# Kernel optimization log

Measured on AMD Instinct MI355X. Metric: run time of the kernel, lower is better.

The kernel has to match this reference:

```python
import jax, jax.numpy as jnp
import numpy as np

B, N, D = 4, 1024, 1024
H, DK, DV = 8, 128, 128
EPS = 1e-6


def setup_inputs() -> dict:
    key = jax.random.key(0)
    ks = jax.random.split(key, 16)
    s = 0.02
    return {
        "q_time": jax.random.normal(ks[0], (B, N, D), jnp.float32),
        "k_time": jax.random.normal(ks[1], (B, N, D), jnp.float32),
        "q_feature": jax.random.normal(ks[2], (B, N, D), jnp.float32),
        "k_feature": jax.random.normal(ks[3], (B, N, D), jnp.float32),
        "v": jax.random.normal(ks[4], (B, N, D), jnp.float32),
        "attn_mask": jax.random.randint(ks[5], (B, N, N), 0, 2, jnp.int32),
        "w_qs_time": jax.random.normal(ks[6], (H * DK, D), jnp.float32) * s,
        "w_ks_time": jax.random.normal(ks[7], (H * DK, D), jnp.float32) * s,
        "w_qs_feature": jax.random.normal(ks[8], (H * DV, D), jnp.float32) * s,
        "w_ks_feature": jax.random.normal(ks[9], (H * DV, D), jnp.float32) * s,
        "w_vs": jax.random.normal(ks[10], (H * DV, D), jnp.float32) * s,
        "w_fc": jax.random.normal(ks[11], (D, H * DV), jnp.float32) * s,
        "ln_gamma": jnp.ones((D,), jnp.float32),
        "ln_beta": jnp.zeros((D,), jnp.float32),
    }


def reference(q_time, k_time, q_feature, k_feature, v, attn_mask,
              w_qs_time, w_ks_time, w_qs_feature, w_ks_feature, w_vs,
              w_fc, ln_gamma, ln_beta):
    temp = DK ** 0.5
    residual = v

    def proj(x, w, d):
        # [B,N,D] @ [D, H*d] -> [B,H,N,d]
        return (x @ w.T).reshape(B, N, H, d).transpose(0, 2, 1, 3)

    qt = proj(q_time, w_qs_time, DK)
    kt = proj(k_time, w_ks_time, DK)
    qf = proj(q_feature, w_qs_feature, DV)
    kf = proj(k_feature, w_ks_feature, DV)
    vv = proj(v, w_vs, DV)

    # time attention: [B,H,N,N]
    attn_time = jnp.einsum('bhnd,bhmd->bhnm', qt / temp, kt)
    attn_time = jnp.where(attn_mask[:, None, :, :] == 0, -1e9, attn_time)
    attn_time = jax.nn.softmax(attn_time, axis=-1)

    # feature attention: q_feature^T @ k_feature -> [B,H,DV,DV]
    attn_feature = jnp.einsum('bhnd,bhne->bhde', qf / temp, kf)
    attn_feature = jax.nn.softmax(attn_feature, axis=-1)

    # chained matmuls: (attn_time @ v) @ attn_feature -> [B,H,N,DV]
    out = jnp.einsum('bhnm,bhmd->bhnd', attn_time, vv)
    out = jnp.einsum('bhnd,bhde->bhne', out, attn_feature)

    out = out.transpose(0, 2, 1, 3).reshape(B, N, H * DV)
    out = out @ w_fc.T + residual  # dropout = identity (eval)

    mean = jnp.mean(out, axis=-1, keepdims=True)
    var = jnp.var(out, axis=-1, keepdims=True)
    out = (out - mean) / jnp.sqrt(var + EPS) * ln_gamma + ln_beta
    return out, attn_time, attn_feature
```

## Files before the change

### kernel.cpp

```cpp
#include <hip/hip_runtime.h>
#include <hip/hip_bf16.h>
#include <cstdint>
#include <cstddef>

typedef unsigned short u16;
typedef unsigned int u32;
typedef short v8s __attribute__((ext_vector_type(8)));
typedef float v4f __attribute__((ext_vector_type(4)));
typedef __hip_bfloat16 bf16;

#define PROJ_ELEMS  4194304ull
#define AT_ELEMS    33554432ull
#define INV_TEMP    0.08838834764831845f

#define GLOBAL_AS __attribute__((address_space(1)))
#define LDS_AS    __attribute__((address_space(3)))

__device__ __forceinline__ void store_out(float* p, float v) { *p = v; }
__device__ __forceinline__ void store_out(bf16* p, float v) { *p = __float2bfloat16(v); }

__device__ __forceinline__ v8s load8f(const float* p) {
    const float4 a = *(const float4*)p;
    const float4 b = *(const float4*)(p + 4);
    v8s r;
    bf16 t;
    t = __float2bfloat16(a.x); r[0] = *(const short*)&t;
    t = __float2bfloat16(a.y); r[1] = *(const short*)&t;
    t = __float2bfloat16(a.z); r[2] = *(const short*)&t;
    t = __float2bfloat16(a.w); r[3] = *(const short*)&t;
    t = __float2bfloat16(b.x); r[4] = *(const short*)&t;
    t = __float2bfloat16(b.y); r[5] = *(const short*)&t;
    t = __float2bfloat16(b.z); r[6] = *(const short*)&t;
    t = __float2bfloat16(b.w); r[7] = *(const short*)&t;
    return r;
}

template <typename AT, typename OutT>
__device__ __forceinline__ void gemm_core(
    const AT* __restrict__ Ab, const u16* __restrict__ Bb, OutT* __restrict__ Cb,
    int K, int lda, int ldb, int ldc, float alpha, int m0, int n0)
{
    __shared__ __align__(16) u16 sA[128][32];
    __shared__ __align__(16) u16 sB[128][32];

    const int tid  = threadIdx.x;
    const int lane = tid & 63;
    const int wid  = tid >> 6;
    const int wm = (wid >> 1) * 64;
    const int wn = (wid & 1) * 64;
    const int quad = lane >> 4;
    const int l16  = lane & 15;

    v4f acc[4][4];
    #pragma unroll
    for (int i = 0; i < 4; ++i)
        #pragma unroll
        for (int j = 0; j < 4; ++j)
            acc[i][j] = (v4f){0.f, 0.f, 0.f, 0.f};

    for (int k0 = 0; k0 < K; k0 += 32) {
        #pragma unroll
        for (int it = 0; it < 2; ++it) {
            const int slot = tid + it * 256;
            const int row  = slot >> 2;
            const int cg   = (slot & 3) << 3;
            __builtin_amdgcn_global_load_lds(
                (const GLOBAL_AS void*)(Bb + (size_t)(n0 + row) * (size_t)ldb + (size_t)(k0 + cg)),
                (LDS_AS void*)((char*)&sB[0][0] + slot * 16), 16, 0, 0);
            if constexpr (sizeof(AT) == 2) {
                __builtin_amdgcn_global_load_lds(
                    (const GLOBAL_AS void*)((const u16*)Ab + (size_t)(m0 + row) * (size_t)lda + (size_t)(k0 + cg)),
                    (LDS_AS void*)((char*)&sA[0][0] + slot * 16), 16, 0, 0);
            } else {
                *(v8s*)&sA[row][cg] =
                    load8f((const float*)Ab + (size_t)(m0 + row) * (size_t)lda + (size_t)(k0 + cg));
            }
        }
        __syncthreads();

        v8s af[4], bfr[4];
        #pragma unroll
        for (int i = 0; i < 4; ++i) {
            af[i]  = *(const v8s*)&sA[wm + i * 16 + l16][quad * 8];
            bfr[i] = *(const v8s*)&sB[wn + i * 16 + l16][quad * 8];
        }
        #pragma unroll
        for (int i = 0; i < 4; ++i)
            #pragma unroll
            for (int j = 0; j < 4; ++j)
                acc[i][j] = __builtin_amdgcn_mfma_f32_16x16x32_bf16(af[i], bfr[j], acc[i][j], 0, 0, 0);
        __syncthreads();
    }

    #pragma unroll
    for (int i = 0; i < 4; ++i) {
        int rbase = m0 + wm + i * 16 + quad * 4;
        #pragma unroll
        for (int j = 0; j < 4; ++j) {
            int gcol = n0 + wn + j * 16 + l16;
            #pragma unroll
            for (int r = 0; r < 4; ++r)
                store_out(&Cb[(size_t)(rbase + r) * (size_t)ldc + (size_t)gcol],
                          acc[i][j][r] * alpha);
        }
    }
}

template <typename AT, typename OutT>
__global__ __launch_bounds__(256, 2)
void gemm_fast(const AT* __restrict__ A, const u16* __restrict__ B, OutT* __restrict__ C,
               int K, int lda, int ldb, int ldc, int batDiv,
               long long sAo, long long sAi, long long sBo, long long sBi,
               long long sCo, long long sCi, float alpha)
{
    const int z  = blockIdx.z;
    const int zo = z / batDiv;
    const int zi = z - zo * batDiv;
    gemm_core<AT, OutT>(A + (size_t)zo * (size_t)sAo + (size_t)zi * (size_t)sAi,
                        B + (size_t)zo * (size_t)sBo + (size_t)zi * (size_t)sBi,
                        C + (size_t)zo * (size_t)sCo + (size_t)zi * (size_t)sCi,
                        K, lda, ldb, ldc, alpha, blockIdx.y * 128, blockIdx.x * 128);
}

struct P5 { const u16* a[5]; };
__global__ __launch_bounds__(256, 2)
void gemm_proj5(P5 As, const u16* __restrict__ W, u16* __restrict__ C)
{
    const int z = blockIdx.z;
    gemm_core<u16, bf16>(As.a[z], W + (size_t)z * 1048576ull,
                         (bf16*)(C + (size_t)z * PROJ_ELEMS),
                         1024, 1024, 1024, 1024, 1.f, blockIdx.y * 128, blockIdx.x * 128);
}

__global__ __launch_bounds__(256, 2)
void gemm_feat_sk(const u16* __restrict__ qfT, const u16* __restrict__ kfT, float* __restrict__ Fp)
{
    const int kc = blockIdx.x, z = blockIdx.y;
    gemm_core<u16, float>(qfT + (size_t)z * 131072ull + (size_t)kc * 128ull,
                          kfT + (size_t)z * 131072ull + (size_t)kc * 128ull,
                          Fp + ((size_t)kc * 32 + z) * 16384ull,
                          128, 1024, 1024, 128, INV_TEMP, 0, 0);
}

template <int NT> struct CP { const float* p[NT]; };

template <int NT>
__global__ __launch_bounds__(256)
void cvt_batch(CP<NT> ps, u16* __restrict__ dst, int perElems)
{
    const float* s = ps.p[blockIdx.z];
    u16* d = dst + (size_t)blockIdx.z * (size_t)perElems;
    const int i = (blockIdx.x * 256 + threadIdx.x) * 8;
    *(v8s*)(d + i) = load8f(s + i);
}

__global__ __launch_bounds__(256)
void mask_pack(const int* __restrict__ mask, u32* __restrict__ mb)
{
    const int w = blockIdx.x * 256 + threadIdx.x;
    const int* src = mask + (size_t)w * 32ull;
    u32 bits = 0;
    #pragma unroll
    for (int i = 0; i < 32; i += 4) {
        int4 v = *(const int4*)(src + i);
        bits |= (u32)(v.x != 0) << i;
        bits |= (u32)(v.y != 0) << (i + 1);
        bits |= (u32)(v.z != 0) << (i + 2);
        bits |= (u32)(v.w != 0) << (i + 3);
    }
    mb[w] = bits;
}

struct T3 { const u16* in[3]; u16* out[3]; };
__global__ __launch_bounds__(256)
void transpose3(T3 t3)
{
    __shared__ u16 tile[32][33];
    const int sel = blockIdx.z >> 5;
    const int z   = blockIdx.z & 31;
    const int b = z >> 3, h = z & 7;
    const u16* ib = t3.in[sel] + (size_t)b * 1048576ull + (size_t)h * 128ull;
    u16* ob = t3.out[sel] + (size_t)z * 131072ull;
    const int m0 = blockIdx.x * 32;
    const int d0 = blockIdx.y * 32;
    const int tx = threadIdx.x;
    const int ty = threadIdx.y;
    #pragma unroll
    for (int i = 0; i < 4; ++i)
        tile[ty + i * 8][tx] = ib[(size_t)(m0 + ty + i * 8) * 1024ull + (size_t)(d0 + tx)];
    __syncthreads();
    #pragma unroll
    for (int i = 0; i < 4; ++i)
        ob[(size_t)(d0 + ty + i * 8) * 1024ull + (size_t)(m0 + tx)] = tile[tx][ty + i * 8];
}

__global__ __launch_bounds__(256, 1)
void fused_attn(const u16* __restrict__ qt, const u16* __restrict__ kt,
                const u16* __restrict__ vvT, const u32* __restrict__ mb,
                float* __restrict__ oAT, u16* __restrict__ opv)
{
    __shared__ __align__(16) u16 sQ[4][128][32];
    __shared__ __align__(16) u16 sK[128][32];
    __shared__ __align__(16) u16 sV[128][32];
    __shared__ __align__(16) u16 sP[4][128][32];
    __shared__ float Mld[128], Lld[128], redT[128];
    __shared__ u32 smw[128][4];

    const int z = blockIdx.y;
    const int b = z >> 3, h = z & 7;
    const int m0 = blockIdx.x * 128;
    const u16* qb = qt + (size_t)b * 1048576ull + (size_t)h * 128ull;
    const u16* kb = kt + (size_t)b * 1048576ull + (size_t)h * 128ull;
    const u16* vb = vvT + (size_t)z * 131072ull;
    float* Ob = oAT + (size_t)z * 1048576ull;
    const u32* mbb = mb + (size_t)b * 32768ull;

    const int tid = threadIdx.x;
    const int lane = tid & 63, wid = tid >> 6;
    const int wm = (wid >> 1) * 64, wn = (wid & 1) * 64;
    const int quad = lane >> 4, l16 = lane & 15;
    const int wnw = wn >> 5;

    if (tid < 128) { Mld[tid] = -3.0e38f; Lld[tid] = 0.f; }

    #pragma unroll
    for (int ks = 0; ks < 4; ++ks)
        #pragma unroll
        for (int it = 0; it < 2; ++it) {
            const int slot = tid + it * 256;
            const int row = slot >> 2, cg = (slot & 3) << 3;
            __builtin_amdgcn_global_load_lds(
                (const GLOBAL_AS void*)(qb + (size_t)(m0 + row) * 1024ull + ks * 32 + cg),
                (LDS_AS void*)((char*)&sQ[ks][0][0] + slot * 16), 16, 0, 0);
        }

    for (int nt = 0; nt < 8; ++nt) {
        v4f acc[4][4];
        #pragma unroll
        for (int i = 0; i < 4; ++i)
            #pragma unroll
            for (int j = 0; j < 4; ++j)
                acc[i][j] = (v4f){0.f, 0.f, 0.f, 0.f};

        #pragma unroll
        for (int ks = 0; ks < 4; ++ks) {
            #pragma unroll
            for (int it = 0; it < 2; ++it) {
                const int slot = tid + it * 256;
                const int row = slot >> 2, cg = (slot & 3) << 3;
                __builtin_amdgcn_global_load_lds(
                    (const GLOBAL_AS void*)(kb + (size_t)(nt * 128 + row) * 1024ull + ks * 32 + cg),
                    (LDS_AS void*)((char*)&sK[0][0] + slot * 16), 16, 0, 0);
            }
            __syncthreads();
            v8s af[4], bfr[4];
            #pragma unroll
            for (int i = 0; i < 4; ++i) {
                af[i]  = *(const v8s*)&sQ[ks][wm + i * 16 + l16][quad * 8];
                bfr[i] = *(const v8s*)&sK[wn + i * 16 + l16][quad * 8];
            }
            #pragma unroll
            for (int i = 0; i < 4; ++i)
                #pragma unroll
                for (int j = 0; j < 4; ++j)
                    acc[i][j] = __builtin_amdgcn_mfma_f32_16x16x32_bf16(af[i], bfr[j], acc[i][j], 0, 0, 0);
            __syncthreads();
        }

        {
            const int row = tid >> 1, w0 = (tid & 1) * 2;
            *(uint2*)&smw[row][w0] = *(const uint2*)(mbb + (size_t)(m0 + row) * 32ull + nt * 4 + w0);
        }
        __syncthreads();

        float tm[4][4];
        #pragma unroll
        for (int i = 0; i < 4; ++i)
            #pragma unroll
            for (int r = 0; r < 4; ++r) {
                tm[i][r] = -3.0e38f;
                const int rowl = wm + i * 16 + quad * 4 + r;
                #pragma unroll
                for (int j = 0; j < 4; ++j) {
                    const u32 word = smw[rowl][wnw + (j >> 1)];
                    const int bit = ((j & 1) << 4) + l16;
                    float s = acc[i][j][r] * INV_TEMP;
                    s = ((word >> bit) & 1u) ? s : -1e9f;
                    acc[i][j][r] = s;
                    tm[i][r] = fmaxf(tm[i][r], s);
                }
                #pragma unroll
                for (int m = 1; m <= 8; m <<= 1)
                    tm[i][r] = fmaxf(tm[i][r], __shfl_xor(tm[i][r], m));
            }

        if ((wid & 1) && l16 == 0) {
            #pragma unroll
            for (int i = 0; i < 4; ++i)
                #pragma unroll
                for (int r = 0; r < 4; ++r)
                    redT[wm + i * 16 + quad * 4 + r] = tm[i][r];
        }
        __syncthreads();

        float scl[4][4];
        if (!(wid & 1) && l16 == 0) {
            #pragma unroll
            for (int i = 0; i < 4; ++i)
                #pragma unroll
                for (int r = 0; r < 4; ++r) {
                    const int rowl = wm + i * 16 + quad * 4 + r;
                    const float full = fmaxf(tm[i][r], redT[rowl]);
                    const float oldM = Mld[rowl];
                    const float newM = fmaxf(oldM, full);
                    Mld[rowl] = newM;
                    scl[i][r] = __expf(oldM - newM);
                }
        }
        __syncthreads();

        float ts[4][4];
        #pragma unroll
        for (int i = 0; i < 4; ++i)
            #pragma unroll
            for (int r = 0; r < 4; ++r) {
                const int rowl = wm + i * 16 + quad * 4 + r;
                const float Mv = Mld[rowl];
                float t = 0.f;
                #pragma unroll
                for (int j = 0; j < 4; ++j)
                    t += __expf(acc[i][j][r] - Mv);
                #pragma unroll
                for (int m = 1; m <= 8; m <<= 1)
                    t += __shfl_xor(t, m);
                ts[i][r] = t;
            }
        if ((wid & 1) && l16 == 0) {
            #pragma unroll
            for (int i = 0; i < 4; ++i)
                #pragma unroll
                for (int r = 0; r < 4; ++r)
                    redT[wm + i * 16 + quad * 4 + r] = ts[i][r];
        }
        __syncthreads();
        if (!(wid & 1) && l16 == 0) {
            #pragma unroll
            for (int i = 0; i < 4; ++i)
                #pragma unroll
                for (int r = 0; r < 4; ++r) {
                    const int rowl = wm + i * 16 + quad * 4 + r;
                    Lld[rowl] = Lld[rowl] * scl[i][r] + ts[i][r] + redT[rowl];
                }
        }
        __syncthreads();
    }

    float Mr[16], IL[16];
    #pragma unroll
    for (int i = 0; i < 4; ++i)
        #pragma unroll
        for (int r = 0; r < 4; ++r) {
            const int rowl = wm + i * 16 + quad * 4 + r;
            Mr[i * 4 + r] = Mld[rowl];
            IL[i * 4 + r] = 1.f / Lld[rowl];
        }

    v4f pacc[4][4];
    #pragma unroll
    for (int i = 0; i < 4; ++i)
        #pragma unroll
        for (int j = 0; j < 4; ++j)
            pacc[i][j] = (v4f){0.f, 0.f, 0.f, 0.f};

    for (int nt = 0; nt < 8; ++nt) {
        v4f acc[4][4];
        #pragma unroll
        for (int i = 0; i < 4; ++i)
            #pragma unroll
            for (int j = 0; j < 4; ++j)
                acc[i][j] = (v4f){0.f, 0.f, 0.f, 0.f};

        #pragma unroll
        for (int ks = 0; ks < 4; ++ks) {
            #pragma unroll
            for (int it = 0; it < 2; ++it) {
                const int slot = tid + it * 256;
                const int row = slot >> 2, cg = (slot & 3) << 3;
                __builtin_amdgcn_global_load_lds(
                    (const GLOBAL_AS void*)(kb + (size_t)(nt * 128 + row) * 1024ull + ks * 32 + cg),
                    (LDS_AS void*)((char*)&sK[0][0] + slot * 16), 16, 0, 0);
            }
            __syncthreads();
            v8s af[4], bfr[4];
            #pragma unroll
            for (int i = 0; i < 4; ++i) {
                af[i]  = *(const v8s*)&sQ[ks][wm + i * 16 + l16][quad * 8];
                bfr[i] = *(const v8s*)&sK[wn + i * 16 + l16][quad * 8];
            }
            #pragma unroll
            for (int i = 0; i < 4; ++i)
                #pragma unroll
                for (int j = 0; j < 4; ++j)
                    acc[i][j] = __builtin_amdgcn_mfma_f32_16x16x32_bf16(af[i], bfr[j], acc[i][j], 0, 0, 0);
            __syncthreads();
        }

        {
            const int row = tid >> 1, w0 = (tid & 1) * 2;
            *(uint2*)&smw[row][w0] = *(const uint2*)(mbb + (size_t)(m0 + row) * 32ull + nt * 4 + w0);
        }
        __syncthreads();

        #pragma unroll
        for (int i = 0; i < 4; ++i)
            #pragma unroll
            for (int r = 0; r < 4; ++r) {
                const int rowl = wm + i * 16 + quad * 4 + r;
                const int idx = i * 4 + r;
                #pragma unroll
                for (int j = 0; j < 4; ++j) {
                    const u32 word = smw[rowl][wnw + (j >> 1)];
                    const int bit = ((j & 1) << 4) + l16;
                    float s = acc[i][j][r] * INV_TEMP;
                    s = ((word >> bit) & 1u) ? s : -1e9f;
                    const float p = __expf(s - Mr[idx]) * IL[idx];
                    const int c = wn + j * 16 + l16;
                    Ob[(size_t)(m0 + rowl) * 1024ull + nt * 128 + c] = p;
                    bf16 pb = __float2bfloat16(p);
                    sP[c >> 5][rowl][c & 31] = *(const u16*)&pb;
                }
            }
        __syncthreads();

        #pragma unroll
        for (int ks = 0; ks < 4; ++ks) {
            #pragma unroll
            for (int it = 0; it < 2; ++it) {
                const int slot = tid + it * 256;
                const int row = slot >> 2, cg = (slot & 3) << 3;
                __builtin_amdgcn_global_load_lds(
                    (const GLOBAL_AS void*)(vb + (size_t)row * 1024ull + nt * 128 + ks * 32 + cg),
                    (LDS_AS void*)((char*)&sV[0][0] + slot * 16), 16, 0, 0);
            }
            __syncthreads();
            v8s af[4], bfr[4];
            #pragma unroll
            for (int i = 0; i < 4; ++i) {
                af[i]  = *(const v8s*)&sP[ks][wm + i * 16 + l16][quad * 8];
                bfr[i] = *(const v8s*)&sV[wn + i * 16 + l16][quad * 8];
            }
            #pragma unroll
            for (int i = 0; i < 4; ++i)
                #pragma unroll
                for (int j = 0; j < 4; ++j)
                    pacc[i][j] = __builtin_amdgcn_mfma_f32_16x16x32_bf16(af[i], bfr[j], pacc[i][j], 0, 0, 0);
            __syncthreads();
        }
    }

    u16* opvB = opv + (size_t)z * 131072ull;
    #pragma unroll
    for (int i = 0; i < 4; ++i) {
        const int rbase = m0 + wm + i * 16 + quad * 4;
        #pragma unroll
        for (int j = 0; j < 4; ++j) {
            const int e = wn + j * 16 + l16;
            #pragma unroll
            for (int r = 0; r < 4; ++r) {
                bf16 t = __float2bfloat16(pacc[i][j][r]);
                opvB[(size_t)(rbase + r) * 128ull + e] = *(const u16*)&t;
            }
        }
    }
}

__global__ __launch_bounds__(128)
void softmax_feat(const float* __restrict__ Fp, float* __restrict__ out_af, u16* __restrict__ FT)
{
    const int r = blockIdx.x;
    const int z = r >> 7, d = r & 127;
    const int e = threadIdx.x;
    float x = 0.f;
    #pragma unroll
    for (int kc = 0; kc < 8; ++kc)
        x += Fp[((size_t)kc * 32 + z) * 16384ull + (size_t)d * 128ull + e];
    float mx = x;
    #pragma unroll
    for (int o = 32; o; o >>= 1) mx = fmaxf(mx, __shfl_xor(mx, o));
    __shared__ float redm[2], reds[2];
    const int w = e >> 6;
    if ((e & 63) == 0) redm[w] = mx;
    __syncthreads();
    mx = fmaxf(redm[0], redm[1]);
    float ex = __expf(x - mx);
    float s = ex;
    #pragma unroll
    for (int o = 32; o; o >>= 1) s += __shfl_xor(s, o);
    if ((e & 63) == 0) reds[w] = s;
    __syncthreads();
    s = reds[0] + reds[1];
    float p = ex / s;
    out_af[(size_t)r * 128ull + e] = p;
    bf16 pb = __float2bfloat16(p);
    FT[(size_t)z * 16384ull + (size_t)e * 128ull + d] = *(const u16*)&pb;
}

__global__ __launch_bounds__(256)
void resid_ln(const float* __restrict__ fc, const float* __restrict__ v,
              const float* __restrict__ gamma, const float* __restrict__ beta,
              float* __restrict__ out)
{
    const int r = blockIdx.x;
    const int t = threadIdx.x;
    const float4* fr = (const float4*)(fc + (size_t)r * 1024ull);
    const float4* vr = (const float4*)(v  + (size_t)r * 1024ull);
    float4 a = fr[t], b4 = vr[t];
    float4 x = {a.x + b4.x, a.y + b4.y, a.z + b4.z, a.w + b4.w};
    float s  = x.x + x.y + x.z + x.w;
    float s2 = x.x * x.x + x.y * x.y + x.z * x.z + x.w * x.w;
    #pragma unroll
    for (int o = 32; o; o >>= 1) { s += __shfl_xor(s, o); s2 += __shfl_xor(s2, o); }
    __shared__ float rs[4], rs2[4];
    const int w = t >> 6;
    if ((t & 63) == 0) { rs[w] = s; rs2[w] = s2; }
    __syncthreads();
    s  = rs[0] + rs[1] + rs[2] + rs[3];
    s2 = rs2[0] + rs2[1] + rs2[2] + rs2[3];
    const float mean = s * (1.f / 1024.f);
    const float var  = s2 * (1.f / 1024.f) - mean * mean;
    const float rstd = rsqrtf(var + 1e-6f);
    const float4 g = ((const float4*)gamma)[t];
    const float4 bb = ((const float4*)beta)[t];
    float4 o4 = {(x.x - mean) * rstd * g.x + bb.x,
                 (x.y - mean) * rstd * g.y + bb.y,
                 (x.z - mean) * rstd * g.z + bb.z,
                 (x.w - mean) * rstd * g.w + bb.w};
    ((float4*)(out + (size_t)r * 1024ull))[t] = o4;
}

extern "C" void kernel_launch(void* const* d_in, const int* in_sizes, int n_in,
                              void* d_out, int out_size, void* d_ws, size_t ws_size,
                              hipStream_t stream)
{
    (void)in_sizes; (void)n_in; (void)out_size; (void)ws_size;
    const float* q_time    = (const float*)d_in[0];
    const float* k_time    = (const float*)d_in[1];
    const float* q_feature = (const float*)d_in[2];
    const float* k_feature = (const float*)d_in[3];
    const float* v_in      = (const float*)d_in[4];
    const int*   mask      = (const int*)d_in[5];
    const float* w_qs_t    = (const float*)d_in[6];
    const float* w_ks_t    = (const float*)d_in[7];
    const float* w_qs_f    = (const float*)d_in[8];
    const float* w_ks_f    = (const float*)d_in[9];
    const float* w_vs      = (const float*)d_in[10];
    const float* w_fc      = (const float*)d_in[11];
    const float* gamma     = (const float*)d_in[12];
    const float* beta      = (const float*)d_in[13];

    char* ws = (char*)d_ws;
    const size_t MB = 1ull << 20;
    u16*   act = (u16*)(ws + 0  * MB);
    u16*   wbf = (u16*)(ws + 40 * MB);
    u16*   qt  = (u16*)(ws + 52 * MB);
    u16*   vvT = (u16*)(ws + 0  * MB);
    u16*   qfT = (u16*)(ws + 8  * MB);
    u16*   kfT = (u16*)(ws + 16 * MB);
    u16*   FT  = (u16*)(ws + 24 * MB);
    float* Fp  = (float*)(ws + 25 * MB);
    u16*   opv = (u16*)(ws + 41 * MB);
    u16*   o2  = (u16*)(ws + 52 * MB);
    float* fc  = (float*)(ws + 60 * MB);
    u32*   mb  = (u32*)(ws + 92 * MB);
    u16*   kt  = qt + PROJ_ELEMS;
    u16*   qf  = kt + PROJ_ELEMS;
    u16*   kf  = qf + PROJ_ELEMS;
    u16*   vv  = kf + PROJ_ELEMS;
    u16*   wfc = wbf + 5ull * 1048576ull;

    float* out0 = (float*)d_out;
    float* oAT  = out0 + PROJ_ELEMS;
    float* oAF  = out0 + PROJ_ELEMS + AT_ELEMS;

    const dim3 blk(256);

    {
        CP<5> ca; ca.p[0] = q_time; ca.p[1] = k_time; ca.p[2] = q_feature;
                  ca.p[3] = k_feature; ca.p[4] = v_in;
        cvt_batch<5><<<dim3(2048, 1, 5), blk, 0, stream>>>(ca, act, 4194304);
        CP<6> cw; cw.p[0] = w_qs_t; cw.p[1] = w_ks_t; cw.p[2] = w_qs_f;
                  cw.p[3] = w_ks_f; cw.p[4] = w_vs; cw.p[5] = w_fc;
        cvt_batch<6><<<dim3(512, 1, 6), blk, 0, stream>>>(cw, wbf, 1048576);
        mask_pack<<<512, blk, 0, stream>>>(mask, mb);
    }

    {
        P5 ps; for (int i = 0; i < 5; ++i) ps.a[i] = act + (size_t)i * PROJ_ELEMS;
        gemm_proj5<<<dim3(8, 32, 5), blk, 0, stream>>>(ps, wbf, qt);
    }

    {
        T3 t3; t3.in[0] = vv; t3.in[1] = qf; t3.in[2] = kf;
               t3.out[0] = vvT; t3.out[1] = qfT; t3.out[2] = kfT;
        transpose3<<<dim3(32, 4, 96), dim3(32, 8, 1), 0, stream>>>(t3);
    }

    gemm_feat_sk<<<dim3(8, 32), blk, 0, stream>>>(qfT, kfT, Fp);

    softmax_feat<<<4096, 128, 0, stream>>>(Fp, oAF, FT);

    fused_attn<<<dim3(8, 32), blk, 0, stream>>>(qt, kt, vvT, mb, oAT, opv);

    gemm_fast<<<dim3(1, 8, 32), blk, 0, stream>>>(opv, FT, (bf16*)o2, 128,
        128, 128, 1024, 8, 1048576LL, 131072LL, 131072LL, 16384LL, 1048576LL, 128LL, 1.f);

    gemm_fast<<<dim3(8, 32, 1), blk, 0, stream>>>(o2, wfc, fc, 1024, 1024, 1024, 1024, 1,
        0LL, 0LL, 0LL, 0LL, 0LL, 0LL, 1.f);

    resid_ln<<<4096, 256, 0, stream>>>(fc, v_in, gamma, beta, out0);
}
```

Baseline: 493.3 us.

## Double-buffer K/V/mask tiles and give each wave full rows for register softmax

```diff
diff --git a/kernel.cpp b/kernel.cpp
--- a/kernel.cpp
+++ b/kernel.cpp
@@ -200,11 +200,9 @@
                 float* __restrict__ oAT, u16* __restrict__ opv)
 {
     __shared__ __align__(16) u16 sQ[4][128][32];
-    __shared__ __align__(16) u16 sK[128][32];
-    __shared__ __align__(16) u16 sV[128][32];
-    __shared__ __align__(16) u16 sP[4][128][32];
-    __shared__ float Mld[128], Lld[128], redT[128];
-    __shared__ u32 smw[128][4];
+    __shared__ __align__(16) u16 sT[2][4][128][32];
+    __shared__ __align__(16) u16 sP[4][128][40];
+    __shared__ u32 smw[2][128][4];
 
     const int z = blockIdx.y;
     const int b = z >> 3, h = z & 7;
@@ -217,254 +215,237 @@
 
     const int tid = threadIdx.x;
     const int lane = tid & 63, wid = tid >> 6;
-    const int wm = (wid >> 1) * 64, wn = (wid & 1) * 64;
     const int quad = lane >> 4, l16 = lane & 15;
-    const int wnw = wn >> 5;
-
-    if (tid < 128) { Mld[tid] = -3.0e38f; Lld[tid] = 0.f; }
-
-    #pragma unroll
-    for (int ks = 0; ks < 4; ++ks)
+    const int wm = wid * 32;
+
+    auto stK = [&](int nt, int buf) {
+        #pragma unroll
+        for (int it = 0; it < 8; ++it) {
+            const int slot = tid + it * 256;
+            const int ks = slot >> 9, row = (slot >> 2) & 127, cg = (slot & 3) << 3;
+            __builtin_amdgcn_global_load_lds(
+                (const GLOBAL_AS void*)(kb + (size_t)(nt * 128 + row) * 1024ull + ks * 32 + cg),
+                (LDS_AS void*)((char*)&sT[buf][0][0][0] + slot * 16), 16, 0, 0);
+        }
+    };
+    auto stV = [&](int nt, int buf) {
+        #pragma unroll
+        for (int it = 0; it < 8; ++it) {
+            const int slot = tid + it * 256;
+            const int ks = slot >> 9, row = (slot >> 2) & 127, cg = (slot & 3) << 3;
+            __builtin_amdgcn_global_load_lds(
+                (const GLOBAL_AS void*)(vb + (size_t)row * 1024ull + nt * 128 + ks * 32 + cg),
+                (LDS_AS void*)((char*)&sT[buf][0][0][0] + slot * 16), 16, 0, 0);
+        }
+    };
+    auto stM = [&](int nt, int buf) {
         #pragma unroll
         for (int it = 0; it < 2; ++it) {
-            const int slot = tid + it * 256;
-            const int row = slot >> 2, cg = (slot & 3) << 3;
+            const int W = wid * 128 + it * 64 + lane;
             __builtin_amdgcn_global_load_lds(
-                (const GLOBAL_AS void*)(qb + (size_t)(m0 + row) * 1024ull + ks * 32 + cg),
-                (LDS_AS void*)((char*)&sQ[ks][0][0] + slot * 16), 16, 0, 0);
-        }
-
+                (const GLOBAL_AS void*)(mbb + (size_t)(m0 + (W >> 2)) * 32ull + nt * 4 + (W & 3)),
+                (LDS_AS void*)((char*)&smw[buf][0][0] + W * 4), 4, 0, 0);
+        }
+    };
+
+    #pragma unroll
+    for (int it = 0; it < 8; ++it) {
+        const int slot = tid + it * 256;
+        const int ks = slot >> 9, row = (slot >> 2) & 127, cg = (slot & 3) << 3;
+        __builtin_amdgcn_global_load_lds(
+            (const GLOBAL_AS void*)(qb + (size_t)(m0 + row) * 1024ull + ks * 32 + cg),
+            (LDS_AS void*)((char*)&sQ[0][0][0] + slot * 16), 16, 0, 0);
+    }
+    stK(0, 0); stM(0, 0);
+
+    float Mreg[8], Lreg[8];
+    #pragma unroll
+    for (int x = 0; x < 8; ++x) { Mreg[x] = -3.0e38f; Lreg[x] = 0.f; }
+
+    int bufA = 0, mcur = 0;
     for (int nt = 0; nt < 8; ++nt) {
-        v4f acc[4][4];
-        #pragma unroll
-        for (int i = 0; i < 4; ++i)
-            #pragma unroll
-            for (int j = 0; j < 4; ++j)
+        stK((nt + 1) & 7, bufA ^ 1);
+        stM((nt + 1) & 7, mcur ^ 1);
+        asm volatile("s_waitcnt vmcnt(10)" ::: "memory");
+        __builtin_amdgcn_s_barrier();
+        __builtin_amdgcn_sched_barrier(0);
+
+        v4f acc[2][8];
+        #pragma unroll
+        for (int i = 0; i < 2; ++i)
+            #pragma unroll
+            for (int j = 0; j < 8; ++j)
                 acc[i][j] = (v4f){0.f, 0.f, 0.f, 0.f};
-
         #pragma unroll
         for (int ks = 0; ks < 4; ++ks) {
-            #pragma unroll
-            for (int it = 0; it < 2; ++it) {
-                const int slot = tid + it * 256;
-                const int row = slot >> 2, cg = (slot & 3) << 3;
-                __builtin_amdgcn_global_load_lds(
-                    (const GLOBAL_AS void*)(kb + (size_t)(nt * 128 + row) * 1024ull + ks * 32 + cg),
-                    (LDS_AS void*)((char*)&sK[0][0] + slot * 16), 16, 0, 0);
-            }
-            __syncthreads();
-            v8s af[4], bfr[4];
-            #pragma unroll
-            for (int i = 0; i < 4; ++i) {
-                af[i]  = *(const v8s*)&sQ[ks][wm + i * 16 + l16][quad * 8];
-                bfr[i] = *(const v8s*)&sK[wn + i * 16 + l16][quad * 8];
-            }
-            #pragma unroll
-            for (int i = 0; i < 4; ++i)
-                #pragma unroll
-                for (int j = 0; j < 4; ++j)
-                    acc[i][j] = __builtin_amdgcn_mfma_f32_16x16x32_bf16(af[i], bfr[j], acc[i][j], 0, 0, 0);
-            __syncthreads();
-        }
-
-        {
-            const int row = tid >> 1, w0 = (tid & 1) * 2;
-            *(uint2*)&smw[row][w0] = *(const uint2*)(mbb + (size_t)(m0 + row) * 32ull + nt * 4 + w0);
-        }
-        __syncthreads();
-
-        float tm[4][4];
-        #pragma unroll
-        for (int i = 0; i < 4; ++i)
+            v8s aq[2], bk[8];
+            #pragma unroll
+            for (int i = 0; i < 2; ++i)
+                aq[i] = *(const v8s*)&sQ[ks][wm + i * 16 + l16][quad * 8];
+            #pragma unroll
+            for (int j = 0; j < 8; ++j)
+                bk[j] = *(const v8s*)&sT[bufA][ks][j * 16 + l16][quad * 8];
+            #pragma unroll
+            for (int i = 0; i < 2; ++i)
+                #pragma unroll
+                for (int j = 0; j < 8; ++j)
+                    acc[i][j] = __builtin_amdgcn_mfma_f32_16x16x32_bf16(aq[i], bk[j], acc[i][j], 0, 0, 0);
+        }
+
+        #pragma unroll
+        for (int i = 0; i < 2; ++i)
             #pragma unroll
             for (int r = 0; r < 4; ++r) {
-                tm[i][r] = -3.0e38f;
+                const int idx = i * 4 + r;
                 const int rowl = wm + i * 16 + quad * 4 + r;
-                #pragma unroll
-                for (int j = 0; j < 4; ++j) {
-                    const u32 word = smw[rowl][wnw + (j >> 1)];
+                const u32 mw0 = smw[mcur][rowl][0];
+                const u32 mw1 = smw[mcur][rowl][1];
+                const u32 mw2 = smw[mcur][rowl][2];
+                const u32 mw3 = smw[mcur][rowl][3];
+                float sv[8];
+                float tmax = -3.0e38f;
+                #pragma unroll
+                for (int j = 0; j < 8; ++j) {
+                    const u32 word = (j < 2) ? mw0 : (j < 4) ? mw1 : (j < 6) ? mw2 : mw3;
                     const int bit = ((j & 1) << 4) + l16;
                     float s = acc[i][j][r] * INV_TEMP;
                     s = ((word >> bit) & 1u) ? s : -1e9f;
-                    acc[i][j][r] = s;
-                    tm[i][r] = fmaxf(tm[i][r], s);
+                    sv[j] = s;
+                    tmax = fmaxf(tmax, s);
                 }
                 #pragma unroll
                 for (int m = 1; m <= 8; m <<= 1)
-                    tm[i][r] = fmaxf(tm[i][r], __shfl_xor(tm[i][r], m));
-            }
-
-        if ((wid & 1) && l16 == 0) {
-            #pragma unroll
-            for (int i = 0; i < 4; ++i)
-                #pragma unroll
-                for (int r = 0; r < 4; ++r)
-                    redT[wm + i * 16 + quad * 4 + r] = tm[i][r];
-        }
-        __syncthreads();
-
-        float scl[4][4];
-        if (!(wid & 1) && l16 == 0) {
-            #pragma unroll
-            for (int i = 0; i < 4; ++i)
-                #pragma unroll
-                for (int r = 0; r < 4; ++r) {
-                    const int rowl = wm + i * 16 + quad * 4 + r;
-                    const float full = fmaxf(tm[i][r], redT[rowl]);
-                    const float oldM = Mld[rowl];
-                    const float newM = fmaxf(oldM, full);
-                    Mld[rowl] = newM;
-                    scl[i][r] = __expf(oldM - newM);
-                }
-        }
-        __syncthreads();
-
-        float ts[4][4];
-        #pragma unroll
-        for (int i = 0; i < 4; ++i)
-            #pragma unroll
-            for (int r = 0; r < 4; ++r) {
-                const int rowl = wm + i * 16 + quad * 4 + r;
-                const float Mv = Mld[rowl];
+                    tmax = fmaxf(tmax, __shfl_xor(tmax, m));
+                const float Mo = Mreg[idx];
+                const float Mn = fmaxf(Mo, tmax);
                 float t = 0.f;
                 #pragma unroll
-                for (int j = 0; j < 4; ++j)
-                    t += __expf(acc[i][j][r] - Mv);
+                for (int j = 0; j < 8; ++j)
+                    t += __expf(sv[j] - Mn);
                 #pragma unroll
                 for (int m = 1; m <= 8; m <<= 1)
                     t += __shfl_xor(t, m);
-                ts[i][r] = t;
+                Lreg[idx] = Lreg[idx] * __expf(Mo - Mn) + t;
+                Mreg[idx] = Mn;
             }
-        if ((wid & 1) && l16 == 0) {
-            #pragma unroll
-            for (int i = 0; i < 4; ++i)
-                #pragma unroll
-                for (int r = 0; r < 4; ++r)
-                    redT[wm + i * 16 + quad * 4 + r] = ts[i][r];
-        }
-        __syncthreads();
-        if (!(wid & 1) && l16 == 0) {
-            #pragma unroll
-            for (int i = 0; i < 4; ++i)
-                #pragma unroll
-                for (int r = 0; r < 4; ++r) {
-                    const int rowl = wm + i * 16 + quad * 4 + r;
-                    Lld[rowl] = Lld[rowl] * scl[i][r] + ts[i][r] + redT[rowl];
-                }
-        }
-        __syncthreads();
-    }
-
-    float Mr[16], IL[16];
-    #pragma unroll
-    for (int i = 0; i < 4; ++i)
-        #pragma unroll
-        for (int r = 0; r < 4; ++r) {
-            const int rowl = wm + i * 16 + quad * 4 + r;
-            Mr[i * 4 + r] = Mld[rowl];
-            IL[i * 4 + r] = 1.f / Lld[rowl];
-        }
-
-    v4f pacc[4][4];
-    #pragma unroll
-    for (int i = 0; i < 4; ++i)
-        #pragma unroll
-        for (int j = 0; j < 4; ++j)
+
+        asm volatile("s_waitcnt lgkmcnt(0)" ::: "memory");
+        __builtin_amdgcn_s_barrier();
+        __builtin_amdgcn_sched_barrier(0);
+        bufA ^= 1; mcur ^= 1;
+    }
+
+    float IL[8];
+    #pragma unroll
+    for (int x = 0; x < 8; ++x) IL[x] = 1.f / Lreg[x];
+
+    const int BK = bufA;
+    const int BV = BK ^ 1;
+
+    v4f pacc[2][8];
+    #pragma unroll
+    for (int i = 0; i < 2; ++i)
+        #pragma unroll
+        for (int j = 0; j < 8; ++j)
             pacc[i][j] = (v4f){0.f, 0.f, 0.f, 0.f};
 
     for (int nt = 0; nt < 8; ++nt) {
-        v4f acc[4][4];
-        #pragma unroll
-        for (int i = 0; i < 4; ++i)
-            #pragma unroll
-            for (int j = 0; j < 4; ++j)
+        stV(nt, BV);
+        asm volatile("s_waitcnt vmcnt(8)" ::: "memory");
+        __builtin_amdgcn_s_barrier();
+        __builtin_amdgcn_sched_barrier(0);
+
+        v4f acc[2][8];
+        #pragma unroll
+        for (int i = 0; i < 2; ++i)
+            #pragma unroll
+            for (int j = 0; j < 8; ++j)
                 acc[i][j] = (v4f){0.f, 0.f, 0.f, 0.f};
-
         #pragma unroll
         for (int ks = 0; ks < 4; ++ks) {
-            #pragma unroll
-            for (int it = 0; it < 2; ++it) {
-                const int slot = tid + it * 256;
-                const int row = slot >> 2, cg = (slot & 3) << 3;
-                __builtin_amdgcn_global_load_lds(
-                    (const GLOBAL_AS void*)(kb + (size_t)(nt * 128 + row) * 1024ull + ks * 32 + cg),
-                    (LDS_AS void*)((char*)&sK[0][0] + slot * 16), 16, 0, 0);
-            }
-            __syncthreads();
-            v8s af[4], bfr[4];
-            #pragma unroll
-            for (int i = 0; i < 4; ++i) {
-                af[i]  = *(const v8s*)&sQ[ks][wm + i * 16 + l16][quad * 8];
-                bfr[i] = *(const v8s*)&sK[wn + i * 16 + l16][quad * 8];
-            }
-            #pragma unroll
-            for (int i = 0; i < 4; ++i)
-                #pragma unroll
-                for (int j = 0; j < 4; ++j)
-                    acc[i][j] = __builtin_amdgcn_mfma_f32_16x16x32_bf16(af[i], bfr[j], acc[i][j], 0, 0, 0);
-            __syncthreads();
-        }
-
-        {
-            const int row = tid >> 1, w0 = (tid & 1) * 2;
-            *(uint2*)&smw[row][w0] = *(const uint2*)(mbb + (size_t)(m0 + row) * 32ull + nt * 4 + w0);
-        }
-        __syncthreads();
-
-        #pragma unroll
-        for (int i = 0; i < 4; ++i)
+            v8s aq[2], bk[8];
+            #pragma unroll
+            for (int i = 0; i < 2; ++i)
+                aq[i] = *(const v8s*)&sQ[ks][wm + i * 16 + l16][quad * 8];
+            #pragma unroll
+            for (int j = 0; j < 8; ++j)
+                bk[j] = *(const v8s*)&sT[BK][ks][j * 16 + l16][quad * 8];
+            #pragma unroll
+            for (int i = 0; i < 2; ++i)
+                #pragma unroll
+                for (int j = 0; j < 8; ++j)
+                    acc[i][j] = __builtin_amdgcn_mfma_f32_16x16x32_bf16(aq[i], bk[j], acc[i][j], 0, 0, 0);
+        }
+
+        asm volatile("s_waitcnt lgkmcnt(0)" ::: "memory");
+        __builtin_amdgcn_s_barrier();
+        __builtin_amdgcn_sched_barrier(0);
+
+        if (nt < 7) {
+            stK(nt + 1, BK);
+            stM(nt + 1, mcur ^ 1);
+            asm volatile("s_waitcnt vmcnt(10)" ::: "memory");
+        } else {
+            asm volatile("s_waitcnt vmcnt(0)" ::: "memory");
+        }
+
+        #pragma unroll
+        for (int i = 0; i < 2; ++i)
             #pragma unroll
             for (int r = 0; r < 4; ++r) {
+                const int idx = i * 4 + r;
                 const int rowl = wm + i * 16 + quad * 4 + r;
-                const int idx = i * 4 + r;
-                #pragma unroll
-                for (int j = 0; j < 4; ++j) {
-                    const u32 word = smw[rowl][wnw + (j >> 1)];
+                const u32 mw0 = smw[mcur][rowl][0];
+                const u32 mw1 = smw[mcur][rowl][1];
+                const u32 mw2 = smw[mcur][rowl][2];
+                const u32 mw3 = smw[mcur][rowl][3];
+                float* orow = Ob + (size_t)(m0 + rowl) * 1024ull + nt * 128;
+                #pragma unroll
+                for (int j = 0; j < 8; ++j) {
+                    const u32 word = (j < 2) ? mw0 : (j < 4) ? mw1 : (j < 6) ? mw2 : mw3;
                     const int bit = ((j & 1) << 4) + l16;
                     float s = acc[i][j][r] * INV_TEMP;
                     s = ((word >> bit) & 1u) ? s : -1e9f;
-                    const float p = __expf(s - Mr[idx]) * IL[idx];
-                    const int c = wn + j * 16 + l16;
-                    Ob[(size_t)(m0 + rowl) * 1024ull + nt * 128 + c] = p;
+                    const float p = __expf(s - Mreg[idx]) * IL[idx];
+                    orow[j * 16 + l16] = p;
                     bf16 pb = __float2bfloat16(p);
-                    sP[c >> 5][rowl][c & 31] = *(const u16*)&pb;
+                    sP[j >> 1][rowl][((j & 1) << 4) + l16] = *(const u16*)&pb;
                 }
             }
-        __syncthreads();
+
+        asm volatile("s_waitcnt lgkmcnt(0)" ::: "memory");
+        __builtin_amdgcn_s_barrier();
+        __builtin_amdgcn_sched_barrier(0);
 
         #pragma unroll
         for (int ks = 0; ks < 4; ++ks) {
-            #pragma unroll
-            for (int it = 0; it < 2; ++it) {
-                const int slot = tid + it * 256;
-                const int row = slot >> 2, cg = (slot & 3) << 3;
-                __builtin_amdgcn_global_load_lds(
-                    (const GLOBAL_AS void*)(vb + (size_t)row * 1024ull + nt * 128 + ks * 32 + cg),
-                    (LDS_AS void*)((char*)&sV[0][0] + slot * 16), 16, 0, 0);
-            }
-            __syncthreads();
-            v8s af[4], bfr[4];
-            #pragma unroll
-            for (int i = 0; i < 4; ++i) {
-                af[i]  = *(const v8s*)&sP[ks][wm + i * 16 + l16][quad * 8];
-                bfr[i] = *(const v8s*)&sV[wn + i * 16 + l16][quad * 8];
-            }
-            #pragma unroll
-            for (int i = 0; i < 4; ++i)
-                #pragma unroll
-                for (int j = 0; j < 4; ++j)
-                    pacc[i][j] = __builtin_amdgcn_mfma_f32_16x16x32_bf16(af[i], bfr[j], pacc[i][j], 0, 0, 0);
-            __syncthreads();
-        }
+            v8s ap[2], bv[8];
+            #pragma unroll
+            for (int i = 0; i < 2; ++i)
+                ap[i] = *(const v8s*)&sP[ks][wm + i * 16 + l16][quad * 8];
+            #pragma unroll
+            for (int j = 0; j < 8; ++j)
+                bv[j] = *(const v8s*)&sT[BV][ks][j * 16 + l16][quad * 8];
+            #pragma unroll
+            for (int i = 0; i < 2; ++i)
+                #pragma unroll
+                for (int j = 0; j < 8; ++j)
+                    pacc[i][j] = __builtin_amdgcn_mfma_f32_16x16x32_bf16(ap[i], bv[j], pacc[i][j], 0, 0, 0);
+        }
+
+        asm volatile("s_waitcnt lgkmcnt(0)" ::: "memory");
+        __builtin_amdgcn_s_barrier();
+        __builtin_amdgcn_sched_barrier(0);
+        mcur ^= 1;
     }
 
     u16* opvB = opv + (size_t)z * 131072ull;
     #pragma unroll
-    for (int i = 0; i < 4; ++i) {
+    for (int i = 0; i < 2; ++i) {
         const int rbase = m0 + wm + i * 16 + quad * 4;
         #pragma unroll
-        for (int j = 0; j < 4; ++j) {
-            const int e = wn + j * 16 + l16;
+        for (int j = 0; j < 8; ++j) {
+            const int e = j * 16 + l16;
             #pragma unroll
             for (int r = 0; r < 4; ++r) {
                 bf16 t = __float2bfloat16(pacc[i][j][r]);
```

Measured after the change: 466.7 us. 5.4% less time.
